# Kernel optimization log

Measured on AMD Instinct MI355X. Metric: run time of the kernel, lower is better.

## Reference

```python
import jax, jax.numpy as jnp
import numpy as np

B, I, O = 262144, 128, 128


def setup_inputs() -> dict:
    key = jax.random.key(0)
    k1, k2, k3, k4 = jax.random.split(key, 4)
    # coordinate-like inputs in [-1, 1]
    x = jax.random.uniform(k1, (B, I), dtype=jnp.float32, minval=-1.0, maxval=1.0)
    # complex weight w = s * exp(i*theta): |w| = s (close to 1 so |w|^x stays stable),
    # angle(w) = theta, matching the torch init where complex_weight = cos(a) + i sin(a).
    theta = jax.random.uniform(k2, (O, I), dtype=jnp.float32, minval=-np.pi, maxval=np.pi)
    scale = jnp.exp(0.1 * jax.random.normal(k3, (O, I), dtype=jnp.float32))
    w_real = scale * jnp.cos(theta)
    w_imag = scale * jnp.sin(theta)
    bias = jax.random.uniform(k4, (O,), dtype=jnp.float32, minval=-np.pi, maxval=np.pi)
    return {"x": x, "w_real": w_real, "w_imag": w_imag, "bias": bias}


def reference(x, w_real, w_imag, bias):
    # complex_weight.abs() and .angle() from real/imag components
    abs_w = jnp.sqrt(w_real * w_real + w_imag * w_imag)      # [O, I]
    angle_w = jnp.arctan2(w_imag, w_real)                     # [O, I]
    # magnitude = prod_i |w|_{o,i} ** x_{b,i}  ==  exp(x @ log|w|^T)
    # (algebraic rewrite of the O(B*O*I) pow+prod into a GEMM + pointwise exp)
    magnitude = jnp.exp(jnp.einsum('bi,oi->bo', x, jnp.log(abs_w)))  # [B, O]
    # y = F.linear(x, angle, bias)
    y = jnp.einsum('bi,oi->bo', x, angle_w) + bias            # [B, O]
    return jnp.cos(y) * magnitude
```

## Files before the change

### kernel.cpp

```cpp
#include <hip/hip_runtime.h>


typedef __attribute__((ext_vector_type(8))) short bf16x8;
typedef __attribute__((ext_vector_type(4))) float f32x4;

#define MFMA(a, b, c) __builtin_amdgcn_mfma_f32_16x16x32_bf16((a), (b), (c), 0, 0, 0)

__device__ __forceinline__ unsigned short f2bf_rne(float f) {
    unsigned u = __float_as_uint(f);
    unsigned r = u + 0x7FFFu + ((u >> 16) & 1u);
    return (unsigned short)(r >> 16);
}

__device__ __forceinline__ void bf16_split(float f, unsigned short& hi, unsigned short& lo) {
    unsigned uh = __float_as_uint(f) & 0xFFFF0000u;
    hi = (unsigned short)(uh >> 16);
    lo = f2bf_rne(f - __uint_as_float(uh));
}

__device__ __forceinline__ void cvt_pair(float f0, float f1, unsigned& h, unsigned& l) {
    unsigned u0 = __float_as_uint(f0), u1 = __float_as_uint(f1);
    unsigned uh0 = u0 & 0xFFFF0000u, uh1 = u1 & 0xFFFF0000u;
    h = (uh0 >> 16) | uh1;
    float r0 = f0 - __uint_as_float(uh0);
    float r1 = f1 - __uint_as_float(uh1);
    unsigned v0 = __float_as_uint(r0), v1 = __float_as_uint(r1);
    v0 = v0 + 0x7FFFu + ((v0 >> 16) & 1u);
    v1 = v1 + 0x7FFFu + ((v1 >> 16) & 1u);
    l = (v0 >> 16) | (v1 & 0xFFFF0000u);
}

__global__ void ces_prep(const float* __restrict__ wr, const float* __restrict__ wi,
                         unsigned short* __restrict__ wsplit) {
    int idx = blockIdx.x * 256 + threadIdx.x;
    float a = wr[idx], b = wi[idx];
    float r2 = a * a + b * b;
    float ang = atan2f(b, a);
    float lg = 0.5f * logf(r2);
    unsigned short ah, al, gh, gl;
    bf16_split(ang, ah, al);
    bf16_split(lg, gh, gl);
    wsplit[idx]         = ah;
    wsplit[16384 + idx] = al;
    wsplit[32768 + idx] = gh;
    wsplit[49152 + idx] = gl;
}

__global__ __launch_bounds__(256, 2) void ces_main(
        const float* __restrict__ x,
        const unsigned short* __restrict__ wsplit,
        const float* __restrict__ bias,
        float* __restrict__ out,
        int ntiles) {
    const int tid  = threadIdx.x;
    const int wave = tid >> 6;
    const int lane = tid & 63;
    const int quad = lane >> 4;
    const int l16  = lane & 15;
    const int n0   = wave * 32;

    bf16x8 wfa_h[2][4], wfa_l[2][4], wfg_h[2][4], wfg_l[2][4];
#pragma unroll
    for (int nt = 0; nt < 2; ++nt) {
        int o = n0 + nt * 16 + l16;
#pragma unroll
        for (int ks = 0; ks < 4; ++ks) {
            int off = o * 128 + ks * 32 + quad * 8;
            wfa_h[nt][ks] = *(const bf16x8*)(wsplit + off);
            wfa_l[nt][ks] = *(const bf16x8*)(wsplit + 16384 + off);
            wfg_h[nt][ks] = *(const bf16x8*)(wsplit + 32768 + off);
            wfg_l[nt][ks] = *(const bf16x8*)(wsplit + 49152 + off);
        }
    }
    float bias_v[2];
    bias_v[0] = bias[n0 + l16];
    bias_v[1] = bias[n0 + 16 + l16];

    const int lo0 = l16 * 128 + quad * 8;

    float4 pf[8];
    {
        const float* xp = x + (size_t)blockIdx.x * (16 * 128);
#pragma unroll
        for (int ks = 0; ks < 4; ++ks) {
            pf[2 * ks]     = *(const float4*)(xp + lo0 + ks * 32);
            pf[2 * ks + 1] = *(const float4*)(xp + lo0 + ks * 32 + 4);
        }
    }

    for (int t = blockIdx.x; t < ntiles; t += gridDim.x) {
        union { unsigned u[4]; bf16x8 v; } ah[4], al[4];
#pragma unroll
        for (int ks = 0; ks < 4; ++ks) {
            cvt_pair(pf[2*ks].x,   pf[2*ks].y,   ah[ks].u[0], al[ks].u[0]);
            cvt_pair(pf[2*ks].z,   pf[2*ks].w,   ah[ks].u[1], al[ks].u[1]);
            cvt_pair(pf[2*ks+1].x, pf[2*ks+1].y, ah[ks].u[2], al[ks].u[2]);
            cvt_pair(pf[2*ks+1].z, pf[2*ks+1].w, ah[ks].u[3], al[ks].u[3]);
        }

        int tn = t + gridDim.x;
        if (tn < ntiles) {
            const float* xp = x + (size_t)tn * (16 * 128);
#pragma unroll
            for (int ks = 0; ks < 4; ++ks) {
                pf[2 * ks]     = *(const float4*)(xp + lo0 + ks * 32);
                pf[2 * ks + 1] = *(const float4*)(xp + lo0 + ks * 32 + 4);
            }
        }

        f32x4 accY[2], accG[2];
        accY[0] = (f32x4){0.f, 0.f, 0.f, 0.f};
        accY[1] = (f32x4){0.f, 0.f, 0.f, 0.f};
        accG[0] = (f32x4){0.f, 0.f, 0.f, 0.f};
        accG[1] = (f32x4){0.f, 0.f, 0.f, 0.f};
#pragma unroll
        for (int ks = 0; ks < 4; ++ks) {
            bf16x8 a_h = ah[ks].v;
            bf16x8 a_l = al[ks].v;
            accY[0] = MFMA(a_h, wfa_h[0][ks], accY[0]);
            accG[0] = MFMA(a_h, wfg_h[0][ks], accG[0]);
            accY[1] = MFMA(a_h, wfa_h[1][ks], accY[1]);
            accG[1] = MFMA(a_h, wfg_h[1][ks], accG[1]);
            accY[0] = MFMA(a_h, wfa_l[0][ks], accY[0]);
            accG[0] = MFMA(a_h, wfg_l[0][ks], accG[0]);
            accY[1] = MFMA(a_h, wfa_l[1][ks], accY[1]);
            accG[1] = MFMA(a_h, wfg_l[1][ks], accG[1]);
            accY[0] = MFMA(a_l, wfa_h[0][ks], accY[0]);
            accG[0] = MFMA(a_l, wfg_h[0][ks], accG[0]);
            accY[1] = MFMA(a_l, wfa_h[1][ks], accY[1]);
            accG[1] = MFMA(a_l, wfg_h[1][ks], accG[1]);
        }

        const int R0 = t * 16;
#pragma unroll
        for (int nt = 0; nt < 2; ++nt) {
            int o = n0 + nt * 16 + l16;
#pragma unroll
            for (int r = 0; r < 4; ++r) {
                float y = accY[nt][r] + bias_v[nt];
                float g = accG[nt][r];
                out[(size_t)(R0 + quad * 4 + r) * 128 + o] = __cosf(y) * __expf(g);
            }
        }
    }
}

extern "C" void kernel_launch(void* const* d_in, const int* in_sizes, int n_in,
                              void* d_out, int out_size, void* d_ws, size_t ws_size,
                              hipStream_t stream) {
    const float* x    = (const float*)d_in[0];
    const float* wr   = (const float*)d_in[1];
    const float* wi   = (const float*)d_in[2];
    const float* bias = (const float*)d_in[3];
    float* out = (float*)d_out;
    unsigned short* wsplit = (unsigned short*)d_ws;

    ces_prep<<<64, 256, 0, stream>>>(wr, wi, wsplit);

    const int B = 262144;
    const int ntiles = B / 16;
    ces_main<<<2048, 256, 0, stream>>>(x, wsplit, bias, out, ntiles);
}
```

Before: 285.7 us.

## Stage bf16-split x tiles in swizzled shared memory, shared across eight waves

Before, each wave loaded and split the whole 16x128 x tile itself. Now a 512-thread block loads each x row tile once, converts it to bf16 hi/lo, and stores it in double-buffered, XOR-swizzled LDS that all eight waves read. Each wave now handles 16 output columns instead of 32, and each block processes a fixed 16 tiles with register prefetch of the next tile. This removes duplicated global loads and conversion work, but adds a __syncthreads per tile and LDS traffic.

```diff
diff --git a/kernel.cpp b/kernel.cpp
--- a/kernel.cpp
+++ b/kernel.cpp
@@ -46,100 +46,95 @@
     wsplit[49152 + idx] = gl;
 }
 
-__global__ __launch_bounds__(256, 2) void ces_main(
+#define NT 16
+
+__global__ __launch_bounds__(512, 4) void ces_main(
         const float* __restrict__ x,
         const unsigned short* __restrict__ wsplit,
         const float* __restrict__ bias,
-        float* __restrict__ out,
-        int ntiles) {
+        float* __restrict__ out) {
+    __shared__ __align__(16) unsigned short smem[8192];
+    char* smemb = (char*)smem;
+
     const int tid  = threadIdx.x;
     const int wave = tid >> 6;
     const int lane = tid & 63;
     const int quad = lane >> 4;
     const int l16  = lane & 15;
-    const int n0   = wave * 32;
+    const int n0   = wave * 16;
 
-    bf16x8 wfa_h[2][4], wfa_l[2][4], wfg_h[2][4], wfg_l[2][4];
-#pragma unroll
-    for (int nt = 0; nt < 2; ++nt) {
-        int o = n0 + nt * 16 + l16;
+    bf16x8 wa_h[4], wa_l[4], wg_h[4], wg_l[4];
+    {
+        const int o = n0 + l16;
 #pragma unroll
         for (int ks = 0; ks < 4; ++ks) {
-            int off = o * 128 + ks * 32 + quad * 8;
-            wfa_h[nt][ks] = *(const bf16x8*)(wsplit + off);
-            wfa_l[nt][ks] = *(const bf16x8*)(wsplit + 16384 + off);
-            wfg_h[nt][ks] = *(const bf16x8*)(wsplit + 32768 + off);
-            wfg_l[nt][ks] = *(const bf16x8*)(wsplit + 49152 + off);
+            const int off = o * 128 + ks * 32 + quad * 8;
+            wa_h[ks] = *(const bf16x8*)(wsplit + off);
+            wa_l[ks] = *(const bf16x8*)(wsplit + 16384 + off);
+            wg_h[ks] = *(const bf16x8*)(wsplit + 32768 + off);
+            wg_l[ks] = *(const bf16x8*)(wsplit + 49152 + off);
         }
     }
-    float bias_v[2];
-    bias_v[0] = bias[n0 + l16];
-    bias_v[1] = bias[n0 + 16 + l16];
+    const float bias_v = bias[n0 + l16];
 
-    const int lo0 = l16 * 128 + quad * 8;
+    const int wrow = tid >> 5;
+    const int wb = (wrow * 256 + (tid & 31) * 8) ^ ((wrow & 7) << 4);
+    int rb[4];
+#pragma unroll
+    for (int ks = 0; ks < 4; ++ks)
+        rb[ks] = (l16 * 256 + ks * 64 + quad * 16) ^ ((l16 & 7) << 4);
 
-    float4 pf[8];
+    const float* xb = x + (size_t)blockIdx.x * (NT * 2048) + tid * 4;
+
     {
-        const float* xp = x + (size_t)blockIdx.x * (16 * 128);
+        float4 v = *(const float4*)xb;
+        unsigned h0, l0, h1, l1;
+        cvt_pair(v.x, v.y, h0, l0);
+        cvt_pair(v.z, v.w, h1, l1);
+        *(uint2*)(smemb + wb)        = make_uint2(h0, h1);
+        *(uint2*)(smemb + wb + 4096) = make_uint2(l0, l1);
+    }
+    float4 pf = *(const float4*)(xb + 2048);
+    __syncthreads();
+
+    for (int i = 0; i < NT; ++i) {
+        const int bo = (i & 1) << 13;
+
+        f32x4 accY = {0.f, 0.f, 0.f, 0.f};
+        f32x4 accG = {0.f, 0.f, 0.f, 0.f};
 #pragma unroll
         for (int ks = 0; ks < 4; ++ks) {
-            pf[2 * ks]     = *(const float4*)(xp + lo0 + ks * 32);
-            pf[2 * ks + 1] = *(const float4*)(xp + lo0 + ks * 32 + 4);
-        }
-    }
-
-    for (int t = blockIdx.x; t < ntiles; t += gridDim.x) {
-        union { unsigned u[4]; bf16x8 v; } ah[4], al[4];
-#pragma unroll
-        for (int ks = 0; ks < 4; ++ks) {
-            cvt_pair(pf[2*ks].x,   pf[2*ks].y,   ah[ks].u[0], al[ks].u[0]);
-            cvt_pair(pf[2*ks].z,   pf[2*ks].w,   ah[ks].u[1], al[ks].u[1]);
-            cvt_pair(pf[2*ks+1].x, pf[2*ks+1].y, ah[ks].u[2], al[ks].u[2]);
-            cvt_pair(pf[2*ks+1].z, pf[2*ks+1].w, ah[ks].u[3], al[ks].u[3]);
+            bf16x8 a_h = *(const bf16x8*)(smemb + (bo + rb[ks]));
+            bf16x8 a_l = *(const bf16x8*)(smemb + (bo + rb[ks] + 4096));
+            accY = MFMA(a_h, wa_h[ks], accY);
+            accG = MFMA(a_h, wg_h[ks], accG);
+            accY = MFMA(a_h, wa_l[ks], accY);
+            accG = MFMA(a_h, wg_l[ks], accG);
+            accY = MFMA(a_l, wa_h[ks], accY);
+            accG = MFMA(a_l, wg_h[ks], accG);
         }
 
-        int tn = t + gridDim.x;
-        if (tn < ntiles) {
-            const float* xp = x + (size_t)tn * (16 * 128);
-#pragma unroll
-            for (int ks = 0; ks < 4; ++ks) {
-                pf[2 * ks]     = *(const float4*)(xp + lo0 + ks * 32);
-                pf[2 * ks + 1] = *(const float4*)(xp + lo0 + ks * 32 + 4);
-            }
+        {
+            const int nbo = bo ^ 8192;
+            unsigned h0, l0, h1, l1;
+            cvt_pair(pf.x, pf.y, h0, l0);
+            cvt_pair(pf.z, pf.w, h1, l1);
+            *(uint2*)(smemb + (nbo + wb))        = make_uint2(h0, h1);
+            *(uint2*)(smemb + (nbo + wb + 4096)) = make_uint2(l0, l1);
         }
+        {
+            int tn = i + 2;
+            if (tn > NT - 1) tn = NT - 1;
+            pf = *(const float4*)(xb + tn * 2048);
+        }
+        __syncthreads();
 
-        f32x4 accY[2], accG[2];
-        accY[0] = (f32x4){0.f, 0.f, 0.f, 0.f};
-        accY[1] = (f32x4){0.f, 0.f, 0.f, 0.f};
-        accG[0] = (f32x4){0.f, 0.f, 0.f, 0.f};
-        accG[1] = (f32x4){0.f, 0.f, 0.f, 0.f};
-#pragma unroll
-        for (int ks = 0; ks < 4; ++ks) {
-            bf16x8 a_h = ah[ks].v;
-            bf16x8 a_l = al[ks].v;
-            accY[0] = MFMA(a_h, wfa_h[0][ks], accY[0]);
-            accG[0] = MFMA(a_h, wfg_h[0][ks], accG[0]);
-            accY[1] = MFMA(a_h, wfa_h[1][ks], accY[1]);
-            accG[1] = MFMA(a_h, wfg_h[1][ks], accG[1]);
-            accY[0] = MFMA(a_h, wfa_l[0][ks], accY[0]);
-            accG[0] = MFMA(a_h, wfg_l[0][ks], accG[0]);
-            accY[1] = MFMA(a_h, wfa_l[1][ks], accY[1]);
-            accG[1] = MFMA(a_h, wfg_l[1][ks], accG[1]);
-            accY[0] = MFMA(a_l, wfa_h[0][ks], accY[0]);
-            accG[0] = MFMA(a_l, wfg_h[0][ks], accG[0]);
-            accY[1] = MFMA(a_l, wfa_h[1][ks], accY[1]);
-            accG[1] = MFMA(a_l, wfg_h[1][ks], accG[1]);
-        }
-
-        const int R0 = t * 16;
-#pragma unroll
-        for (int nt = 0; nt < 2; ++nt) {
-            int o = n0 + nt * 16 + l16;
+        {
+            float* op = out + ((size_t)(blockIdx.x * NT + i) * 16 + quad * 4) * 128 + n0 + l16;
 #pragma unroll
             for (int r = 0; r < 4; ++r) {
-                float y = accY[nt][r] + bias_v[nt];
-                float g = accG[nt][r];
-                out[(size_t)(R0 + quad * 4 + r) * 128 + o] = __cosf(y) * __expf(g);
+                float y = accY[r] + bias_v;
+                op[(size_t)r * 128] = __cosf(y) * __expf(accG[r]);
             }
         }
     }
@@ -157,7 +152,5 @@
 
     ces_prep<<<64, 256, 0, stream>>>(wr, wi, wsplit);
 
-    const int B = 262144;
-    const int ntiles = B / 16;
-    ces_main<<<2048, 256, 0, stream>>>(x, wsplit, bias, out, ntiles);
+    ces_main<<<1024, 512, 0, stream>>>(x, wsplit, bias, out);
 }
```

Result: faster. 252.7 us (-11.6%).
